# Kernel optimization log

Hardware: AMD Instinct MI355X
Metric: run time of the kernel (lower is better)

## Reference

```python
import jax, jax.numpy as jnp
import numpy as np

N_NODES = 50000
N_EDGES = 600000
D_IN = 128
D = 128
N_REL = 2
N_LAYERS = 3


def rgcn_conv(h, src, dst, edge_type, weight, root, bias):
    # PyG RGCNConv (no bases), aggr='mean' per relation:
    # out_i = h_i @ root + bias + sum_r mean_{j in N_r(i)} h_j @ W_r
    out = h @ root + bias                      # [N, D]
    hs = h[src]                                # [E, D] gather once
    for r in range(N_REL):
        mask = (edge_type == r).astype(h.dtype)          # [E]
        agg = jax.ops.segment_sum(hs * mask[:, None], dst, num_segments=N_NODES)  # [N, D]
        cnt = jax.ops.segment_sum(mask, dst, num_segments=N_NODES)                # [N]
        mean = agg / jnp.maximum(cnt, 1.0)[:, None]
        out = out + mean @ weight[r]
    return out


def setup_inputs() -> dict:
    key = jax.random.key(0)
    ks = jax.random.split(key, 10)
    x = jax.random.normal(ks[0], (N_NODES, D_IN), dtype=jnp.float32)
    edge_index = jax.random.randint(ks[1], (2, N_EDGES), 0, N_NODES, dtype=jnp.int64)
    edge_attr = jax.random.normal(ks[2], (N_EDGES, N_REL), dtype=jnp.float32)
    # input projection f: Linear(D_IN, D); stored as [D_IN, D] (apply as x @ Wf + bf)
    Wf = jax.random.normal(ks[3], (D_IN, D), dtype=jnp.float32) / np.sqrt(D_IN)
    bf = jnp.zeros((D,), dtype=jnp.float32)
    # per-layer RGCNConv params, stacked over layers
    conv_weight = jax.random.normal(ks[4], (N_LAYERS, N_REL, D, D), dtype=jnp.float32) / np.sqrt(D)
    conv_root = jax.random.normal(ks[5], (N_LAYERS, D, D), dtype=jnp.float32) / np.sqrt(D)
    conv_bias = jnp.zeros((N_LAYERS, D), dtype=jnp.float32)
    return {"x": x, "edge_index": edge_index, "edge_attr": edge_attr,
            "Wf": Wf, "bf": bf, "conv_weight": conv_weight,
            "conv_root": conv_root, "conv_bias": conv_bias}


def reference(x, edge_index, edge_attr, Wf, bf, conv_weight, conv_root, conv_bias):
    src, dst = edge_index[0], edge_index[1]
    edge_type = jnp.argmax(edge_attr, axis=1)           # [E]
    h = jax.nn.relu(x @ Wf + bf)                        # [N, D]
    for l in range(N_LAYERS):
        h = rgcn_conv(h, src, dst, edge_type, conv_weight[l], conv_root[l], conv_bias[l])
        h = jax.nn.relu(h)
    return h
```

## Files before the change

### kernel.cpp

```cpp
#include <hip/hip_runtime.h>
#include <hip/hip_bf16.h>

#define NN 50000
#define NE 600000
#define D 128
#define NREL 2
#define BM 128

typedef __attribute__((ext_vector_type(8))) short bf16x8;
typedef __attribute__((ext_vector_type(4))) float f32x4;

__device__ __forceinline__ float bf2f(short s) {
    return __uint_as_float(((unsigned int)(unsigned short)s) << 16);
}
__device__ __forceinline__ bf16x8 pack_bf8(const float* a) {
    union { bf16x8 v; __hip_bfloat162 h2[4]; } o;
#pragma unroll
    for (int i = 0; i < 4; i++)
        o.h2[i] = __float22bfloat162_rn(make_float2(a[2 * i], a[2 * i + 1]));
    return o.v;
}

#define NEB ((NE + 255) / 256)
#define NWT (16384 + 3 * 49152)
#define NWB ((NWT + 255) / 256)

__global__ void k_pre1(const float* __restrict__ attr,
                       const int* __restrict__ dst,
                       int* __restrict__ cnt,
                       const float* __restrict__ Wf,
                       const float* __restrict__ cw,
                       const float* __restrict__ cr,
                       __hip_bfloat16* __restrict__ wt) {
    if (blockIdx.x < NEB) {
        int i = blockIdx.x * blockDim.x + threadIdx.x;
        if (i >= NE) return;
        float2 a = reinterpret_cast<const float2*>(attr)[i];
        int r = (a.y > a.x) ? 1 : 0;
        atomicAdd(&cnt[r * NN + dst[i]], 1);
    } else {
        int idx = (blockIdx.x - NEB) * blockDim.x + threadIdx.x;
        if (idx >= NWT) return;
        float v;
        if (idx < 16384) {
            int n = idx >> 7, k = idx & 127;
            v = Wf[k * 128 + n];
        } else {
            int j = idx - 16384;
            int l = j / 49152; j %= 49152;
            int n = j / 384, k = j % 384;
            if (k < 128)      v = cr[((size_t)l * 128 + k) * 128 + n];
            else if (k < 256) v = cw[((size_t)(l * 2 + 0) * 128 + (k - 128)) * 128 + n];
            else              v = cw[((size_t)(l * 2 + 1) * 128 + (k - 256)) * 128 + n];
        }
        wt[idx] = __float2bfloat16(v);
    }
}

__global__ void k_pre2(const int* __restrict__ cnt, float* __restrict__ inv,
                       int* __restrict__ off, int* __restrict__ cur,
                       int* __restrict__ total) {
    int i = blockIdx.x * blockDim.x + threadIdx.x;
    if (i >= NREL * NN) return;
    int c = cnt[i];
    inv[i] = 1.0f / (float)(c > 1 ? c : 1);
    int o = atomicAdd(total, c);
    off[i] = o;
    cur[i] = o;
}

__global__ void k_fill(const float* __restrict__ attr,
                       const int* __restrict__ src, const int* __restrict__ dst,
                       int* __restrict__ cursor, int* __restrict__ srcs, int E) {
    int i = blockIdx.x * blockDim.x + threadIdx.x;
    if (i >= E) return;
    float2 a = reinterpret_cast<const float2*>(attr)[i];
    int r = (a.y > a.x) ? 1 : 0;
    int pos = atomicAdd(&cursor[r * NN + dst[i]], 1);
    srcs[pos] = src[i];
}

__global__ __launch_bounds__(256)
void k_aggregate(const __hip_bfloat16* __restrict__ h,
                 const int* __restrict__ srcs,
                 const int* __restrict__ off, const int* __restrict__ cnt,
                 const float* __restrict__ inv,
                 __hip_bfloat16* __restrict__ agg) {
    int wid = (blockIdx.x * blockDim.x + threadIdx.x) >> 6;
    int lane = threadIdx.x & 63;
    if (wid >= NREL * NN) return;
    int start = off[wid], c = cnt[wid];
    int g = lane >> 4, l16 = lane & 15;

    int sv = (lane < c) ? srcs[start + lane] : 0;

    float acc[8];
#pragma unroll
    for (int i = 0; i < 8; i++) acc[i] = 0.f;

    for (int base = 0; base < c; base += 16) {
        int s[4];
#pragma unroll
        for (int q = 0; q < 4; q++) {
            int jj = base + g + q * 4;
            int t = __shfl(sv, jj & 63);
            s[q] = (jj < 64) ? t : ((jj < c) ? srcs[start + jj] : 0);
            if (jj >= c) s[q] = 0;
        }
        bf16x8 v[4];
#pragma unroll
        for (int q = 0; q < 4; q++)
            v[q] = *reinterpret_cast<const bf16x8*>(h + (size_t)s[q] * D + l16 * 8);
#pragma unroll
        for (int q = 0; q < 4; q++) {
            bool ok = (base + g + q * 4) < c;
#pragma unroll
            for (int i = 0; i < 8; i++) acc[i] += ok ? bf2f(v[q][i]) : 0.f;
        }
    }

#pragma unroll
    for (int i = 0; i < 8; i++) acc[i] += __shfl_xor(acc[i], 16);
#pragma unroll
    for (int i = 0; i < 8; i++) acc[i] += __shfl_xor(acc[i], 32);

    if (g == 0) {
        float sc = inv[wid];
        float t[8];
#pragma unroll
        for (int i = 0; i < 8; i++) t[i] = acc[i] * sc;
        *reinterpret_cast<bf16x8*>(agg + (size_t)wid * D + l16 * 8) = pack_bf8(t);
    }
}

__global__ __launch_bounds__(256)
void k_gemm_proj(const float* __restrict__ X,
                 const __hip_bfloat16* __restrict__ Wt,
                 const float* __restrict__ bias,
                 __hip_bfloat16* __restrict__ out, int N) {
    __shared__ uint4 sB4[1024];
    char* sB = (char*)sB4;
    const int tid = threadIdx.x;
    const int w = tid >> 6;
    const int l16 = tid & 15, lg = (tid & 63) >> 4;

    f32x4 acc[2][8];
#pragma unroll
    for (int m = 0; m < 2; m++)
#pragma unroll
        for (int n = 0; n < 8; n++) acc[m][n] = (f32x4)(0.f);

    const int row0 = blockIdx.x * 128;
#pragma unroll
    for (int kb = 0; kb < 2; ++kb) {
        bf16x8 afr[2][2];
#pragma unroll
        for (int mb = 0; mb < 2; ++mb)
#pragma unroll
            for (int kk = 0; kk < 2; ++kk) {
                int r = row0 + w * 32 + mb * 16 + l16;
                if (r >= N) r = N - 1;
                const float* p = X + (size_t)r * D + kb * 64 + kk * 32 + lg * 8;
                float4 u0 = reinterpret_cast<const float4*>(p)[0];
                float4 u1 = reinterpret_cast<const float4*>(p)[1];
                float t[8] = {u0.x, u0.y, u0.z, u0.w, u1.x, u1.y, u1.z, u1.w};
                afr[mb][kk] = pack_bf8(t);
            }
        __syncthreads();
        {
            int trow = tid >> 3, tb = (tid & 7) * 16;
#pragma unroll
            for (int p = 0; p < 4; ++p) {
                int rr = trow + p * 32;
                uint4 v = *reinterpret_cast<const uint4*>(
                    (const char*)(Wt + (size_t)rr * 128 + kb * 64) + tb);
                *reinterpret_cast<uint4*>(sB + rr * 128 + (tb ^ ((rr & 7) << 4))) = v;
            }
        }
        __syncthreads();
#pragma unroll
        for (int kk = 0; kk < 2; ++kk)
#pragma unroll
            for (int nb = 0; nb < 8; ++nb) {
                int brow = nb * 16 + l16;
                int bcol = kk * 64 + lg * 16;
                bf16x8 bfr = *reinterpret_cast<const bf16x8*>(
                    sB + brow * 128 + (bcol ^ ((brow & 7) << 4)));
                acc[0][nb] = __builtin_amdgcn_mfma_f32_16x16x32_bf16(
                    afr[0][kk], bfr, acc[0][nb], 0, 0, 0);
                acc[1][nb] = __builtin_amdgcn_mfma_f32_16x16x32_bf16(
                    afr[1][kk], bfr, acc[1][nb], 0, 0, 0);
            }
    }
#pragma unroll
    for (int nb = 0; nb < 8; ++nb) {
        int n = nb * 16 + l16;
        float bv = bias[n];
#pragma unroll
        for (int mb = 0; mb < 2; ++mb)
#pragma unroll
            for (int r = 0; r < 4; ++r) {
                int grow = row0 + w * 32 + mb * 16 + lg * 4 + r;
                if (grow < N) {
                    float v = acc[mb][nb][r] + bv;
                    v = v > 0.f ? v : 0.f;
                    out[(size_t)grow * D + n] = __float2bfloat16(v);
                }
            }
    }
}

template <int KTOT, bool OUT_F32>
__global__ __launch_bounds__(256)
void k_gemm_mfma(const __hip_bfloat16* __restrict__ A0,
                 const __hip_bfloat16* __restrict__ A1,
                 const __hip_bfloat16* __restrict__ A2,
                 const __hip_bfloat16* __restrict__ Wt,
                 const float* __restrict__ bias,
                 void* __restrict__ outv, int N) {
    __shared__ uint4 sB4[1024];
    char* sB = (char*)sB4;
    const int tid = threadIdx.x;
    const int w = tid >> 6;
    const int l16 = tid & 15, lg = (tid & 63) >> 4;
    const __hip_bfloat16* As[3] = {A0, A1, A2};

    f32x4 acc[2][8];
#pragma unroll
    for (int m = 0; m < 2; m++)
#pragma unroll
        for (int n = 0; n < 8; n++) acc[m][n] = (f32x4)(0.f);

    const size_t row0 = (size_t)blockIdx.x * BM;
    const int NKB = KTOT / 64;
#pragma unroll
    for (int kb = 0; kb < NKB; ++kb) {
        const __hip_bfloat16* Ac = As[kb >> 1];
        const int koff = (kb & 1) * 64;
        bf16x8 afr[2][2];
#pragma unroll
        for (int mb = 0; mb < 2; ++mb)
#pragma unroll
            for (int kk = 0; kk < 2; ++kk) {
                int r = (int)row0 + w * 32 + mb * 16 + l16;
                if (r >= N) r = N - 1;
                afr[mb][kk] = *reinterpret_cast<const bf16x8*>(
                    Ac + (size_t)r * D + koff + kk * 32 + lg * 8);
            }
        __syncthreads();
        {
            int trow = tid >> 3;
            int tb = (tid & 7) * 16;
#pragma unroll
            for (int p = 0; p < 4; ++p) {
                int rr = trow + p * 32;
                uint4 v = *reinterpret_cast<const uint4*>(
                    (const char*)(Wt + (size_t)rr * KTOT + kb * 64) + tb);
                *reinterpret_cast<uint4*>(sB + rr * 128 + (tb ^ ((rr & 7) << 4))) = v;
            }
        }
        __syncthreads();
#pragma unroll
        for (int kk = 0; kk < 2; ++kk) {
#pragma unroll
            for (int nb = 0; nb < 8; ++nb) {
                int brow = nb * 16 + l16;
                int bcol = kk * 64 + lg * 16;
                bf16x8 bfr = *reinterpret_cast<const bf16x8*>(
                    sB + brow * 128 + (bcol ^ ((brow & 7) << 4)));
                acc[0][nb] = __builtin_amdgcn_mfma_f32_16x16x32_bf16(
                    afr[0][kk], bfr, acc[0][nb], 0, 0, 0);
                acc[1][nb] = __builtin_amdgcn_mfma_f32_16x16x32_bf16(
                    afr[1][kk], bfr, acc[1][nb], 0, 0, 0);
            }
        }
    }
#pragma unroll
    for (int nb = 0; nb < 8; ++nb) {
        int n = nb * 16 + l16;
        float bv = bias[n];
#pragma unroll
        for (int mb = 0; mb < 2; ++mb) {
#pragma unroll
            for (int r = 0; r < 4; ++r) {
                long grow = (long)row0 + w * 32 + mb * 16 + lg * 4 + r;
                if (grow < N) {
                    float v = acc[mb][nb][r] + bv;
                    v = v > 0.f ? v : 0.f;
                    if (OUT_F32)
                        ((float*)outv)[(size_t)grow * D + n] = v;
                    else
                        ((__hip_bfloat16*)outv)[(size_t)grow * D + n] =
                            __float2bfloat16(v);
                }
            }
        }
    }
}

extern "C" void kernel_launch(void* const* d_in, const int* in_sizes, int n_in,
                              void* d_out, int out_size, void* d_ws, size_t ws_size,
                              hipStream_t stream) {
    const float* x    = (const float*)d_in[0];
    const int*   ei   = (const int*)d_in[1];
    const float* attr = (const float*)d_in[2];
    const float* Wf   = (const float*)d_in[3];
    const float* bf   = (const float*)d_in[4];
    const float* cw   = (const float*)d_in[5];
    const float* cr   = (const float*)d_in[6];
    const float* cb   = (const float*)d_in[7];
    const int* src  = ei;
    const int* dstv = ei + NE;

    char* p = (char*)d_ws;
    __hip_bfloat16* h0   = (__hip_bfloat16*)p; p += (size_t)NN * D * 2;
    __hip_bfloat16* h1   = (__hip_bfloat16*)p; p += (size_t)NN * D * 2;
    __hip_bfloat16* aggb = (__hip_bfloat16*)p; p += (size_t)2 * NN * D * 2;
    __hip_bfloat16* wt   = (__hip_bfloat16*)p; p += (size_t)NWT * 2;
    float* inv  = (float*)p;                p += (size_t)2 * NN * 4;
    int*   cnt  = (int*)p;                  p += (size_t)2 * NN * 4;
    int*   off  = (int*)p;                  p += (size_t)2 * NN * 4;
    int*   cur  = (int*)p;                  p += (size_t)2 * NN * 4;
    int*   srcs = (int*)p;                  p += (size_t)NE * 4;
    int*   total= (int*)p;

    float* outp = (float*)d_out;

    hipMemsetAsync(cnt, 0, (size_t)2 * NN * sizeof(int), stream);
    hipMemsetAsync(total, 0, sizeof(int), stream);
    k_pre1<<<NEB + NWB, 256, 0, stream>>>(attr, dstv, cnt, Wf, cw, cr, wt);
    k_pre2<<<(2 * NN + 255) / 256, 256, 0, stream>>>(cnt, inv, off, cur, total);
    k_fill<<<NEB, 256, 0, stream>>>(attr, src, dstv, cur, srcs, NE);

    k_gemm_proj<<<(NN + 127) / 128, 256, 0, stream>>>(x, wt, bf, h0, NN);

    const int gblocks = (NN + BM - 1) / BM;
    const int ablocks = (2 * NN * 64 + 255) / 256;
    for (int l = 0; l < 3; ++l) {
        const __hip_bfloat16* hin = (l == 1) ? h1 : h0;
        k_aggregate<<<ablocks, 256, 0, stream>>>(hin, srcs, off, cnt, inv, aggb);
        const __hip_bfloat16* wl = wt + 16384 + (size_t)l * 49152;
        const float* bl = cb + (size_t)l * D;
        if (l == 2) {
            k_gemm_mfma<384, true><<<gblocks, 256, 0, stream>>>(
                hin, aggb, aggb + (size_t)NN * D, wl, bl, outp, NN);
        } else {
            __hip_bfloat16* hout = (l == 0) ? h1 : h0;
            k_gemm_mfma<384, false><<<gblocks, 256, 0, stream>>>(
                hin, aggb, aggb + (size_t)NN * D, wl, bl, hout, NN);
        }
    }
}
```

Measured before the change: 271.1 us.

## Interleave per-relation CSR by node and aggregate both relations per wavefront

The count and cursor arrays move from a relation-major to a node-interleaved layout, so each destination node's edges for both relations sit contiguously in the CSR. The aggregation kernel now uses one wavefront per node, handling both relations in a single pass with two accumulators, and writes a combined [N,256] aggregate. The GEMM reads that interleaved aggregate through per-operand strides. The aim is to halve the number of wavefronts and to make better use of the 64-lane prefetch of source indices, which typically covers around 12 edges per node instead of about 6 per relation, at the cost of doubled accumulator registers.

```diff
diff --git a/kernel.cpp b/kernel.cpp
--- a/kernel.cpp
+++ b/kernel.cpp
@@ -37,7 +37,7 @@
         if (i >= NE) return;
         float2 a = reinterpret_cast<const float2*>(attr)[i];
         int r = (a.y > a.x) ? 1 : 0;
-        atomicAdd(&cnt[r * NN + dst[i]], 1);
+        atomicAdd(&cnt[dst[i] * 2 + r], 1);
     } else {
         int idx = (blockIdx.x - NEB) * blockDim.x + threadIdx.x;
         if (idx >= NWT) return;
@@ -61,12 +61,13 @@
                        int* __restrict__ off, int* __restrict__ cur,
                        int* __restrict__ total) {
     int i = blockIdx.x * blockDim.x + threadIdx.x;
-    if (i >= NREL * NN) return;
-    int c = cnt[i];
-    inv[i] = 1.0f / (float)(c > 1 ? c : 1);
-    int o = atomicAdd(total, c);
-    off[i] = o;
-    cur[i] = o;
+    if (i >= NN) return;
+    int c0 = cnt[2 * i], c1 = cnt[2 * i + 1];
+    inv[2 * i]     = 1.0f / (float)(c0 > 1 ? c0 : 1);
+    inv[2 * i + 1] = 1.0f / (float)(c1 > 1 ? c1 : 1);
+    int o = atomicAdd(total, c0 + c1);
+    off[2 * i] = o;       cur[2 * i] = o;
+    off[2 * i + 1] = o + c0; cur[2 * i + 1] = o + c0;
 }
 
 __global__ void k_fill(const float* __restrict__ attr,
@@ -76,7 +77,7 @@
     if (i >= E) return;
     float2 a = reinterpret_cast<const float2*>(attr)[i];
     int r = (a.y > a.x) ? 1 : 0;
-    int pos = atomicAdd(&cursor[r * NN + dst[i]], 1);
+    int pos = atomicAdd(&cursor[dst[i] * 2 + r], 1);
     srcs[pos] = src[i];
 }
 
@@ -86,50 +87,93 @@
                  const int* __restrict__ off, const int* __restrict__ cnt,
                  const float* __restrict__ inv,
                  __hip_bfloat16* __restrict__ agg) {
-    int wid = (blockIdx.x * blockDim.x + threadIdx.x) >> 6;
+    int node = (blockIdx.x * blockDim.x + threadIdx.x) >> 6;
     int lane = threadIdx.x & 63;
-    if (wid >= NREL * NN) return;
-    int start = off[wid], c = cnt[wid];
+    if (node >= NN) return;
+    int st = off[2 * node];
+    int c0 = cnt[2 * node], c01 = c0 + cnt[2 * node + 1];
     int g = lane >> 4, l16 = lane & 15;
 
-    int sv = (lane < c) ? srcs[start + lane] : 0;
-
-    float acc[8];
-#pragma unroll
-    for (int i = 0; i < 8; i++) acc[i] = 0.f;
-
-    for (int base = 0; base < c; base += 16) {
-        int s[4];
-#pragma unroll
-        for (int q = 0; q < 4; q++) {
-            int jj = base + g + q * 4;
-            int t = __shfl(sv, jj & 63);
-            s[q] = (jj < 64) ? t : ((jj < c) ? srcs[start + jj] : 0);
-            if (jj >= c) s[q] = 0;
-        }
-        bf16x8 v[4];
-#pragma unroll
-        for (int q = 0; q < 4; q++)
-            v[q] = *reinterpret_cast<const bf16x8*>(h + (size_t)s[q] * D + l16 * 8);
-#pragma unroll
-        for (int q = 0; q < 4; q++) {
-            bool ok = (base + g + q * 4) < c;
-#pragma unroll
-            for (int i = 0; i < 8; i++) acc[i] += ok ? bf2f(v[q][i]) : 0.f;
-        }
-    }
-
-#pragma unroll
-    for (int i = 0; i < 8; i++) acc[i] += __shfl_xor(acc[i], 16);
-#pragma unroll
-    for (int i = 0; i < 8; i++) acc[i] += __shfl_xor(acc[i], 32);
+    int sv = (lane < c01) ? srcs[st + lane] : 0;
+
+    float acc0[8], acc1[8];
+#pragma unroll
+    for (int i = 0; i < 8; i++) { acc0[i] = 0.f; acc1[i] = 0.f; }
+
+    if (c01 <= 64) {
+        for (int base = 0; base < c01; base += 16) {
+            int s[4]; int jj[4];
+#pragma unroll
+            for (int q = 0; q < 4; q++) {
+                jj[q] = base + g + q * 4;
+                int t = __shfl(sv, jj[q] & 63);
+                s[q] = (jj[q] < c01) ? t : 0;
+            }
+            bf16x8 v[4];
+#pragma unroll
+            for (int q = 0; q < 4; q++)
+                v[q] = *reinterpret_cast<const bf16x8*>(
+                    h + (size_t)s[q] * D + l16 * 8);
+#pragma unroll
+            for (int q = 0; q < 4; q++) {
+                bool ok0 = jj[q] < c0;
+                bool ok1 = !ok0 && (jj[q] < c01);
+#pragma unroll
+                for (int i = 0; i < 8; i++) {
+                    float f = bf2f(v[q][i]);
+                    acc0[i] += ok0 ? f : 0.f;
+                    acc1[i] += ok1 ? f : 0.f;
+                }
+            }
+        }
+    } else {
+        for (int base = 0; base < c01; base += 16) {
+            int s[4]; int jj[4];
+#pragma unroll
+            for (int q = 0; q < 4; q++) {
+                jj[q] = base + g + q * 4;
+                int t = __shfl(sv, jj[q] & 63);
+                s[q] = (jj[q] < 64) ? t : ((jj[q] < c01) ? srcs[st + jj[q]] : 0);
+                if (jj[q] >= c01) s[q] = 0;
+            }
+            bf16x8 v[4];
+#pragma unroll
+            for (int q = 0; q < 4; q++)
+                v[q] = *reinterpret_cast<const bf16x8*>(
+                    h + (size_t)s[q] * D + l16 * 8);
+#pragma unroll
+            for (int q = 0; q < 4; q++) {
+                bool ok0 = jj[q] < c0;
+                bool ok1 = !ok0 && (jj[q] < c01);
+#pragma unroll
+                for (int i = 0; i < 8; i++) {
+                    float f = bf2f(v[q][i]);
+                    acc0[i] += ok0 ? f : 0.f;
+                    acc1[i] += ok1 ? f : 0.f;
+                }
+            }
+        }
+    }
+
+#pragma unroll
+    for (int i = 0; i < 8; i++) {
+        acc0[i] += __shfl_xor(acc0[i], 16);
+        acc1[i] += __shfl_xor(acc1[i], 16);
+    }
+#pragma unroll
+    for (int i = 0; i < 8; i++) {
+        acc0[i] += __shfl_xor(acc0[i], 32);
+        acc1[i] += __shfl_xor(acc1[i], 32);
+    }
 
     if (g == 0) {
-        float sc = inv[wid];
-        float t[8];
-#pragma unroll
-        for (int i = 0; i < 8; i++) t[i] = acc[i] * sc;
-        *reinterpret_cast<bf16x8*>(agg + (size_t)wid * D + l16 * 8) = pack_bf8(t);
+        float s0 = inv[2 * node], s1 = inv[2 * node + 1];
+        float t0[8], t1[8];
+#pragma unroll
+        for (int i = 0; i < 8; i++) { t0[i] = acc0[i] * s0; t1[i] = acc1[i] * s1; }
+        __hip_bfloat16* dstp = agg + (size_t)node * 256;
+        *reinterpret_cast<bf16x8*>(dstp + l16 * 8)       = pack_bf8(t0);
+        *reinterpret_cast<bf16x8*>(dstp + 128 + l16 * 8) = pack_bf8(t1);
     }
 }
 
@@ -210,11 +254,11 @@
     }
 }
 
-template <int KTOT, bool OUT_F32>
+template <bool OUT_F32>
 __global__ __launch_bounds__(256)
-void k_gemm_mfma(const __hip_bfloat16* __restrict__ A0,
-                 const __hip_bfloat16* __restrict__ A1,
-                 const __hip_bfloat16* __restrict__ A2,
+void k_gemm_mfma(const __hip_bfloat16* __restrict__ A0, int sA0,
+                 const __hip_bfloat16* __restrict__ A1, int sA1,
+                 const __hip_bfloat16* __restrict__ A2, int sA2,
                  const __hip_bfloat16* __restrict__ Wt,
                  const float* __restrict__ bias,
                  void* __restrict__ outv, int N) {
@@ -224,6 +268,7 @@
     const int w = tid >> 6;
     const int l16 = tid & 15, lg = (tid & 63) >> 4;
     const __hip_bfloat16* As[3] = {A0, A1, A2};
+    const int strides[3] = {sA0, sA1, sA2};
 
     f32x4 acc[2][8];
 #pragma unroll
@@ -232,10 +277,10 @@
         for (int n = 0; n < 8; n++) acc[m][n] = (f32x4)(0.f);
 
     const size_t row0 = (size_t)blockIdx.x * BM;
-    const int NKB = KTOT / 64;
-#pragma unroll
-    for (int kb = 0; kb < NKB; ++kb) {
+#pragma unroll
+    for (int kb = 0; kb < 6; ++kb) {
         const __hip_bfloat16* Ac = As[kb >> 1];
+        const int strideC = strides[kb >> 1];
         const int koff = (kb & 1) * 64;
         bf16x8 afr[2][2];
 #pragma unroll
@@ -245,7 +290,7 @@
                 int r = (int)row0 + w * 32 + mb * 16 + l16;
                 if (r >= N) r = N - 1;
                 afr[mb][kk] = *reinterpret_cast<const bf16x8*>(
-                    Ac + (size_t)r * D + koff + kk * 32 + lg * 8);
+                    Ac + (size_t)r * strideC + koff + kk * 32 + lg * 8);
             }
         __syncthreads();
         {
@@ -255,7 +300,7 @@
             for (int p = 0; p < 4; ++p) {
                 int rr = trow + p * 32;
                 uint4 v = *reinterpret_cast<const uint4*>(
-                    (const char*)(Wt + (size_t)rr * KTOT + kb * 64) + tb);
+                    (const char*)(Wt + (size_t)rr * 384 + kb * 64) + tb);
                 *reinterpret_cast<uint4*>(sB + rr * 128 + (tb ^ ((rr & 7) << 4))) = v;
             }
         }
@@ -329,25 +374,25 @@
     hipMemsetAsync(cnt, 0, (size_t)2 * NN * sizeof(int), stream);
     hipMemsetAsync(total, 0, sizeof(int), stream);
     k_pre1<<<NEB + NWB, 256, 0, stream>>>(attr, dstv, cnt, Wf, cw, cr, wt);
-    k_pre2<<<(2 * NN + 255) / 256, 256, 0, stream>>>(cnt, inv, off, cur, total);
+    k_pre2<<<(NN + 255) / 256, 256, 0, stream>>>(cnt, inv, off, cur, total);
     k_fill<<<NEB, 256, 0, stream>>>(attr, src, dstv, cur, srcs, NE);
 
     k_gemm_proj<<<(NN + 127) / 128, 256, 0, stream>>>(x, wt, bf, h0, NN);
 
     const int gblocks = (NN + BM - 1) / BM;
-    const int ablocks = (2 * NN * 64 + 255) / 256;
+    const int ablocks = (NN * 64 + 255) / 256;
     for (int l = 0; l < 3; ++l) {
         const __hip_bfloat16* hin = (l == 1) ? h1 : h0;
         k_aggregate<<<ablocks, 256, 0, stream>>>(hin, srcs, off, cnt, inv, aggb);
         const __hip_bfloat16* wl = wt + 16384 + (size_t)l * 49152;
         const float* bl = cb + (size_t)l * D;
         if (l == 2) {
-            k_gemm_mfma<384, true><<<gblocks, 256, 0, stream>>>(
-                hin, aggb, aggb + (size_t)NN * D, wl, bl, outp, NN);
+            k_gemm_mfma<true><<<gblocks, 256, 0, stream>>>(
+                hin, 128, aggb, 256, aggb + 128, 256, wl, bl, outp, NN);
         } else {
             __hip_bfloat16* hout = (l == 0) ? h1 : h0;
-            k_gemm_mfma<384, false><<<gblocks, 256, 0, stream>>>(
-                hin, aggb, aggb + (size_t)NN * D, wl, bl, hout, NN);
-        }
-    }
-}
+            k_gemm_mfma<false><<<gblocks, 256, 0, stream>>>(
+                hin, 128, aggb, 256, aggb + 128, 256, wl, bl, hout, NN);
+        }
+    }
+}
```

After: 269.1 us. Within noise of the previous version (-0.7%).
